# Optimization experiments

Hardware: AMD Instinct MI355X
Metric: run time of the kernel (lower is better)

The kernel has to match this reference:

```python
import jax, jax.numpy as jnp
import numpy as np

F = 256       # in_src/in_dst feature dim (feat_dict)
HID = 256     # hidden_dim
K = 16        # sampled neighbors per dst node (fixed fan-out)
N_REVIEW = 16384
N_USER = 65536
N_PRODUCT = 65536
EPS = 1e-5


def setup_inputs() -> dict:
    key = jax.random.key(0)
    ks = jax.random.split(key, 24)
    rn = lambda k, shape, s=0.05: jax.random.normal(k, shape, jnp.float32) * s
    inp = {
        'x_user': jax.random.normal(ks[0], (N_USER, F), jnp.float32),
        'x_product': jax.random.normal(ks[1], (N_PRODUCT, F), jnp.float32),
        'x_review': jax.random.normal(ks[2], (N_REVIEW, F), jnp.float32),
        'nbr_user': jax.random.randint(ks[3], (N_REVIEW, K), 0, N_USER),
        'nbr_product': jax.random.randint(ks[4], (N_REVIEW, K), 0, N_PRODUCT),
    }
    i = 5
    for pre in ('u_', 'p_'):
        inp[pre + 'Wih'] = rn(ks[i], (4 * F, F)); i += 1      # LSTM input weights (gates i,f,g,o)
        inp[pre + 'Whh'] = rn(ks[i], (4 * F, F)); i += 1      # LSTM hidden weights
        inp[pre + 'bih'] = jnp.zeros((4 * F,), jnp.float32)
        inp[pre + 'bhh'] = jnp.zeros((4 * F,), jnp.float32)
        inp[pre + 'Wself'] = rn(ks[i], (HID, F)); i += 1      # SAGEConv fc_self
        inp[pre + 'Wneigh'] = rn(ks[i], (HID, F)); i += 1     # SAGEConv fc_neigh
        inp[pre + 'bconv'] = jnp.zeros((HID,), jnp.float32)   # SAGEConv bias
    inp['ln_g'] = jnp.ones((HID,), jnp.float32)
    inp['ln_b'] = jnp.zeros((HID,), jnp.float32)
    inp['bn_g'] = jnp.ones((HID,), jnp.float32)
    inp['bn_b'] = jnp.zeros((HID,), jnp.float32)
    inp['W1'] = rn(ks[i], (HID, HID)); i += 1
    inp['b1'] = jnp.zeros((HID,), jnp.float32)
    inp['W2'] = rn(ks[i], (2, HID)); i += 1
    inp['b2'] = jnp.zeros((2,), jnp.float32)
    return inp


def _lstm_last(x, Wih, Whh, bih, bhh):
    # x: [N, K, F] neighbor sequences; returns final hidden state [N, F]
    n, _, f = x.shape
    b = bih + bhh
    def step(carry, xt):  # xt: [N, F]
        h, c = carry
        gates = xt @ Wih.T + h @ Whh.T + b  # [N, 4F]
        ig, fg, gg, og = jnp.split(gates, 4, axis=-1)
        c = jax.nn.sigmoid(fg) * c + jax.nn.sigmoid(ig) * jnp.tanh(gg)
        h = jax.nn.sigmoid(og) * jnp.tanh(c)
        return (h, c), None
    h0 = jnp.zeros((n, f), x.dtype)
    (h, _), _ = jax.lax.scan(step, (h0, h0), jnp.swapaxes(x, 0, 1))
    return h


def _sage_rel(x_src, x_dst, nbr, Wih, Whh, bih, bhh, Wself, Wneigh, bconv):
    # gather neighbor features [N_dst, K, F] (feat_drop is identity at eval)
    nb = x_src[nbr]
    h_neigh = _lstm_last(nb, Wih, Whh, bih, bhh)            # [N_dst, F]
    rst = x_dst @ Wself.T + h_neigh @ Wneigh.T + bconv       # [N_dst, HID]
    return jax.nn.gelu(rst, approximate=False)               # activation=nn.GELU()


def reference(x_user, x_product, x_review, nbr_user, nbr_product,
              u_Wih, u_Whh, u_bih, u_bhh, u_Wself, u_Wneigh, u_bconv,
              p_Wih, p_Whh, p_bih, p_bhh, p_Wself, p_Wneigh, p_bconv,
              ln_g, ln_b, bn_g, bn_b, W1, b1, W2, b2):
    # HeteroGraphConv(aggregate='sum') over the two relations into 'review'
    h = (_sage_rel(x_user, x_review, nbr_user, u_Wih, u_Whh, u_bih, u_bhh,
                   u_Wself, u_Wneigh, u_bconv)
         + _sage_rel(x_product, x_review, nbr_product, p_Wih, p_Whh, p_bih, p_bhh,
                     p_Wself, p_Wneigh, p_bconv))
    # LayerNorm
    mu = jnp.mean(h, axis=-1, keepdims=True)
    var = jnp.var(h, axis=-1, keepdims=True)
    h = (h - mu) * jax.lax.rsqrt(var + EPS) * ln_g + ln_b
    # clf head: Dropout (identity at eval) -> BatchNorm1d (batch stats) -> MLP
    bm = jnp.mean(h, axis=0, keepdims=True)
    bv = jnp.var(h, axis=0, keepdims=True)
    h = (h - bm) * jax.lax.rsqrt(bv + EPS) * bn_g + bn_b
    h = jax.nn.gelu(h @ W1.T + b1, approximate=False)
    return h @ W2.T + b2  # [N_REVIEW, 2]
```

## Files before the change

### kernel.cpp

```cpp
#include <hip/hip_runtime.h>
#include <math.h>

#define NREV 16384
#define NUSER 65536
#define NPROD 65536
#define KNBR 16
#define LDK 72

typedef __attribute__((ext_vector_type(8))) short short8;
typedef __attribute__((ext_vector_type(4))) float f32x4;
typedef unsigned short u16;

__device__ __forceinline__ u16 f2bf(float f){
  union { float f; unsigned u; } x; x.f = f;
  unsigned r = x.u + 0x7fffu + ((x.u >> 16) & 1u);
  return (u16)(r >> 16);
}
__device__ __forceinline__ float bf2f(u16 u){
  union { unsigned u; float f; } x; x.u = ((unsigned)u) << 16;
  return x.f;
}
__device__ __forceinline__ float fexp2(float x){ return __builtin_amdgcn_exp2f(x); }
__device__ __forceinline__ float frcp(float x){ return __builtin_amdgcn_rcpf(x); }
#define LOG2E 1.4426950408889634f
__device__ __forceinline__ float sigf(float x){ return frcp(1.f + fexp2(-LOG2E*x)); }
__device__ __forceinline__ float tanh_fast(float x){ return 1.f - 2.f*frcp(1.f + fexp2(2.f*LOG2E*x)); }
__device__ __forceinline__ float gelu_fast(float x){
  float u = 0.7978845608f*x*(1.f + 0.044715f*x*x);
  return 0.5f*x*(1.f + tanh_fast(u));
}

__global__ void cvt_kernel(const float* __restrict__ src, u16* __restrict__ dst, int n4){
  int i = blockIdx.x*256 + threadIdx.x;
  if(i < n4){
    float4 v = reinterpret_cast<const float4*>(src)[i];
    ushort4 o; o.x=f2bf(v.x); o.y=f2bf(v.y); o.z=f2bf(v.z); o.w=f2bf(v.w);
    reinterpret_cast<ushort4*>(dst)[i] = o;
  }
}

__global__ void pack_lstm_kernel(const float* __restrict__ Wihp, const float* __restrict__ Whhp,
                                 const float* __restrict__ bihp, const float* __restrict__ bhhp,
                                 u16* __restrict__ Bpp, float* __restrict__ bpp){
  int n = blockIdx.x;
  int g = n & 3, j = n >> 2;
  int m = g*256 + j;
  int k = threadIdx.x;
  Bpp[(size_t)n*512 + k]       = f2bf(Wihp[(size_t)m*256 + k]);
  Bpp[(size_t)n*512 + 256 + k] = f2bf(Whhp[(size_t)m*256 + k]);
  if(k == 0) bpp[n] = bihp[m] + bhhp[m];
}

__global__ void pack_sage_kernel(const float* __restrict__ Wselfp, const float* __restrict__ Wneighp,
                                 u16* __restrict__ Bsp){
  int n = blockIdx.x;
  int k = threadIdx.x;
  Bsp[(size_t)n*512 + k]       = f2bf(Wselfp[(size_t)n*256 + k]);
  Bsp[(size_t)n*512 + 256 + k] = f2bf(Wneighp[(size_t)n*256 + k]);
}

__global__ __launch_bounds__(256) void xw_kernel(
    const float* __restrict__ x, const u16* __restrict__ Bp,
    const float* __restrict__ bp, u16* __restrict__ xwout)
{
  __shared__ u16 sA[128*LDK];
  __shared__ u16 sB[128*LDK];
  int tid = threadIdx.x;
  int nt = blockIdx.x, rt = blockIdx.y;
  f32x4 acc[4][4];
  #pragma unroll
  for(int i=0;i<4;++i)
    #pragma unroll
    for(int j=0;j<4;++j) acc[i][j] = (f32x4){0.f,0.f,0.f,0.f};
  int lane = tid & 63, w = tid >> 6, wr = w >> 1, wc = w & 1;
  int ci = tid & 7, r0 = tid >> 3;
  int rrow = lane & 15, kb = (lane >> 4) * 8;

  for(int kt=0; kt<4; ++kt){
    __syncthreads();
    #pragma unroll
    for(int pp=0; pp<4; ++pp){
      int row = pp*32 + r0;
      const float* srcA = x + (size_t)(rt*128 + row)*256 + kt*64 + ci*8;
      float4 a0 = *(const float4*)srcA;
      float4 a1 = *(const float4*)(srcA + 4);
      short8 s;
      s[0]=f2bf(a0.x); s[1]=f2bf(a0.y); s[2]=f2bf(a0.z); s[3]=f2bf(a0.w);
      s[4]=f2bf(a1.x); s[5]=f2bf(a1.y); s[6]=f2bf(a1.z); s[7]=f2bf(a1.w);
      *(short8*)&sA[row*LDK + ci*8] = s;
      const u16* srcB = Bp + (size_t)(nt*128 + row)*512 + kt*64;
      *(short8*)&sB[row*LDK + ci*8] = *(const short8*)(srcB + ci*8);
    }
    __syncthreads();
    #pragma unroll
    for(int kk=0; kk<2; ++kk){
      short8 af[4], bfv[4];
      #pragma unroll
      for(int ni=0;ni<4;++ni) af[ni]  = *(const short8*)&sB[(wc*64+ni*16+rrow)*LDK + kk*32 + kb];
      #pragma unroll
      for(int mi=0;mi<4;++mi) bfv[mi] = *(const short8*)&sA[(wr*64+mi*16+rrow)*LDK + kk*32 + kb];
      #pragma unroll
      for(int ni=0;ni<4;++ni)
        #pragma unroll
        for(int mi=0;mi<4;++mi)
          acc[ni][mi] = __builtin_amdgcn_mfma_f32_16x16x32_bf16(af[ni], bfv[mi], acc[ni][mi], 0, 0, 0);
    }
  }
  #pragma unroll
  for(int mi=0;mi<4;++mi){
    size_t node = (size_t)(rt*128 + wr*64 + mi*16 + rrow);
    u16* dst = xwout + node*1024;
    #pragma unroll
    for(int ni=0;ni<4;++ni){
      int n0 = nt*128 + wc*64 + ni*16 + (lane>>4)*4;
      float4 bv = *(const float4*)&bp[n0];
      ushort4 o;
      o.x = f2bf(acc[ni][mi][0] + bv.x);
      o.y = f2bf(acc[ni][mi][1] + bv.y);
      o.z = f2bf(acc[ni][mi][2] + bv.z);
      o.w = f2bf(acc[ni][mi][3] + bv.w);
      *(ushort4*)(dst + n0) = o;
    }
  }
}

__global__ __launch_bounds__(256, 3) void lstm_step3_kernel(
    const u16* __restrict__ xw, const int* __restrict__ nbr, int t,
    const u16* __restrict__ Bh,
    const u16* __restrict__ hin, u16* __restrict__ hout, float* __restrict__ cT)
{
  __shared__ u16 sA[128*LDK];
  __shared__ u16 sB[128*LDK];
  int tid = threadIdx.x;
  int rt = blockIdx.x, nt = blockIdx.y;
  int lane = tid & 63, w = tid >> 6, wr = w >> 1, wc = w & 1;
  int ci = tid & 7, r0 = tid >> 3;
  int rrow = lane & 15, lhi = lane >> 4, kb = lhi * 8;

  int node[4];
  #pragma unroll
  for(int mi=0;mi<4;++mi)
    node[mi] = nbr[(size_t)(rt*128 + wr*64 + mi*16 + rrow)*KNBR + t];
  ushort4 xv[4][4];
  #pragma unroll
  for(int mi=0;mi<4;++mi)
    #pragma unroll
    for(int ni=0;ni<4;++ni){
      int n0 = nt*128 + wc*64 + ni*16 + lhi*4;
      xv[mi][ni] = *(const ushort4*)(xw + (size_t)node[mi]*1024 + n0);
    }

  f32x4 acc[4][4];
  #pragma unroll
  for(int i=0;i<4;++i)
    #pragma unroll
    for(int j=0;j<4;++j) acc[i][j] = (f32x4){0.f,0.f,0.f,0.f};

  if(t > 0){
    for(int kt=0; kt<4; ++kt){
      __syncthreads();
      #pragma unroll
      for(int pp=0; pp<4; ++pp){
        int row = pp*32 + r0;
        *(short8*)&sA[row*LDK + ci*8] =
          *(const short8*)(hin + (size_t)(rt*128 + row)*256 + kt*64 + ci*8);
        *(short8*)&sB[row*LDK + ci*8] =
          *(const short8*)(Bh + (size_t)(nt*128 + row)*512 + kt*64 + ci*8);
      }
      __syncthreads();
      #pragma unroll
      for(int kk=0; kk<2; ++kk){
        short8 af[4], bfv[4];
        #pragma unroll
        for(int ni=0;ni<4;++ni) af[ni]  = *(const short8*)&sB[(wc*64+ni*16+rrow)*LDK + kk*32 + kb];
        #pragma unroll
        for(int mi=0;mi<4;++mi) bfv[mi] = *(const short8*)&sA[(wr*64+mi*16+rrow)*LDK + kk*32 + kb];
        #pragma unroll
        for(int ni=0;ni<4;++ni)
          #pragma unroll
          for(int mi=0;mi<4;++mi)
            acc[ni][mi] = __builtin_amdgcn_mfma_f32_16x16x32_bf16(af[ni], bfv[mi], acc[ni][mi], 0, 0, 0);
      }
    }
  }

  float cvv[4][4];
  #pragma unroll
  for(int mi=0;mi<4;++mi)
    #pragma unroll
    for(int ni=0;ni<4;++ni){
      cvv[mi][ni] = 0.f;
      if(t > 0){
        int j = nt*32 + wc*16 + ni*4 + lhi;
        cvv[mi][ni] = cT[(size_t)j*NREV + rt*128 + wr*64 + mi*16 + rrow];
      }
    }

  #pragma unroll
  for(int mi=0;mi<4;++mi){
    int rg = rt*128 + wr*64 + mi*16 + rrow;
    #pragma unroll
    for(int ni=0;ni<4;++ni){
      int j = nt*32 + wc*16 + ni*4 + lhi;
      float ig = bf2f(xv[mi][ni].x) + acc[ni][mi][0];
      float fg = bf2f(xv[mi][ni].y) + acc[ni][mi][1];
      float gg = bf2f(xv[mi][ni].z) + acc[ni][mi][2];
      float og = bf2f(xv[mi][ni].w) + acc[ni][mi][3];
      float cn = sigf(fg)*cvv[mi][ni] + sigf(ig)*tanh_fast(gg);
      cT[(size_t)j*NREV + rg] = cn;
      hout[(size_t)rg*256 + j] = f2bf(sigf(og)*tanh_fast(cn));
    }
  }
}

template<int MODE>
__global__ __launch_bounds__(256) void gemm_act_kernel(
    const u16* __restrict__ A0, const u16* __restrict__ A1,
    const u16* __restrict__ Bp, const float* __restrict__ bias,
    float* __restrict__ outF, u16* __restrict__ outH)
{
  constexpr int KT   = (MODE == 2) ? 4 : 8;
  constexpr int KTOT = KT * 64;
  __shared__ u16 sA[128*LDK];
  __shared__ u16 sB[128*LDK];
  int tid = threadIdx.x;
  int rt = blockIdx.x, nt = blockIdx.y;
  f32x4 acc[4][4];
  #pragma unroll
  for(int i=0;i<4;++i)
    #pragma unroll
    for(int j=0;j<4;++j) acc[i][j] = (f32x4){0.f,0.f,0.f,0.f};
  int lane = tid & 63, w = tid >> 6, wr = w >> 1, wc = w & 1;
  int ci = tid & 7, r0 = tid >> 3;
  int rrow = lane & 15, kb = (lane >> 4) * 8;

  for(int kt=0; kt<KT; ++kt){
    __syncthreads();
    #pragma unroll
    for(int pp=0; pp<4; ++pp){
      int row = pp*32 + r0;
      const u16* srcA = (kt < 4)
        ? (A0 + ((size_t)(rt*128 + row))*256 + kt*64)
        : (A1 + ((size_t)(rt*128 + row))*256 + (kt-4)*64);
      *(short8*)&sA[row*LDK + ci*8] = *(const short8*)(srcA + ci*8);
      const u16* srcB = Bp + ((size_t)(nt*128 + row))*KTOT + kt*64;
      *(short8*)&sB[row*LDK + ci*8] = *(const short8*)(srcB + ci*8);
    }
    __syncthreads();
    #pragma unroll
    for(int kk=0; kk<2; ++kk){
      short8 af[4], bfv[4];
      #pragma unroll
      for(int mi=0;mi<4;++mi) af[mi] = *(const short8*)&sA[(wr*64+mi*16+rrow)*LDK + kk*32 + kb];
      #pragma unroll
      for(int ni=0;ni<4;++ni) bfv[ni] = *(const short8*)&sB[(wc*64+ni*16+rrow)*LDK + kk*32 + kb];
      #pragma unroll
      for(int mi=0;mi<4;++mi)
        #pragma unroll
        for(int ni=0;ni<4;++ni)
          acc[mi][ni] = __builtin_amdgcn_mfma_f32_16x16x32_bf16(af[mi], bfv[ni], acc[mi][ni], 0, 0, 0);
    }
  }
  #pragma unroll
  for(int mi=0;mi<4;++mi)
    #pragma unroll
    for(int ni=0;ni<4;++ni){
      int col  = nt*128 + wc*64 + ni*16 + rrow;
      int rowb = rt*128 + wr*64 + mi*16 + (lane>>4)*4;
      float bv = bias[col];
      #pragma unroll
      for(int q=0;q<4;++q){
        float x = acc[mi][ni][q] + bv;
        float gl = gelu_fast(x);
        size_t idx = (size_t)(rowb+q)*256 + col;
        if(MODE == 0)      outF[idx] = gl;
        else if(MODE == 1) outF[idx] += gl;
        else               outH[idx] = f2bf(gl);
      }
    }
}

__global__ void ln_kernel(const float* __restrict__ hs, const float* __restrict__ g,
                          const float* __restrict__ b, u16* __restrict__ hlnp){
  int w = threadIdx.x >> 6, lane = threadIdx.x & 63;
  int r = blockIdx.x*4 + w;
  const float* row = hs + (size_t)r*256;
  float4 v = *(const float4*)(row + lane*4);
  float s  = v.x+v.y+v.z+v.w;
  float ss = v.x*v.x + v.y*v.y + v.z*v.z + v.w*v.w;
  #pragma unroll
  for(int d=1; d<64; d<<=1){ s += __shfl_xor(s, d, 64); ss += __shfl_xor(ss, d, 64); }
  float mu  = s  * (1.f/256.f);
  float var = ss * (1.f/256.f) - mu*mu;
  float rs  = rsqrtf(var + 1e-5f);
  float4 gv = *(const float4*)(g + lane*4);
  float4 bv = *(const float4*)(b + lane*4);
  ushort4 o;
  o.x = f2bf((v.x-mu)*rs*gv.x + bv.x);
  o.y = f2bf((v.y-mu)*rs*gv.y + bv.y);
  o.z = f2bf((v.z-mu)*rs*gv.z + bv.z);
  o.w = f2bf((v.w-mu)*rs*gv.w + bv.w);
  *(ushort4*)(hlnp + (size_t)r*256 + lane*4) = o;
}

__global__ void colstats_kernel(const u16* __restrict__ hlnp, float* __restrict__ cs, float* __restrict__ cq){
  int cix = threadIdx.x;
  size_t rb = (size_t)blockIdx.x * 128;
  float s=0.f, q=0.f;
  for(int rr=0; rr<128; ++rr){
    float v = bf2f(hlnp[(rb+rr)*256 + cix]);
    s += v; q += v*v;
  }
  atomicAdd(&cs[cix], s);
  atomicAdd(&cq[cix], q);
}

__global__ void fold_kernel(const float* __restrict__ cs, const float* __restrict__ cq,
                            const float* __restrict__ bng, const float* __restrict__ bnb,
                            const float* __restrict__ W1p, const float* __restrict__ b1p,
                            u16* __restrict__ W1fp, float* __restrict__ b1fp){
  __shared__ float sS[256], sT[256];
  int cix = threadIdx.x;
  float bm = cs[cix] * (1.f/16384.f);
  float bv = cq[cix] * (1.f/16384.f) - bm*bm;
  float s  = bng[cix] * rsqrtf(bv + 1e-5f);
  float tt = bnb[cix] - bm*s;
  sS[cix]=s; sT[cix]=tt;
  __syncthreads();
  float a = b1p[cix];
  for(int k=0;k<256;++k){
    float wv = W1p[(size_t)cix*256 + k];
    W1fp[(size_t)cix*256 + k] = f2bf(wv * sS[k]);
    a += wv * sT[k];
  }
  b1fp[cix] = a;
}

__global__ void head_kernel(const u16* __restrict__ z, const float* __restrict__ W2p,
                            const float* __restrict__ b2p, float* __restrict__ outp){
  int w = threadIdx.x >> 6, lane = threadIdx.x & 63;
  int r = blockIdx.x*4 + w;
  const u16* zr = z + (size_t)r*256;
  ushort4 v = *(const ushort4*)(zr + lane*4);
  float z0=bf2f(v.x), z1v=bf2f(v.y), z2=bf2f(v.z), z3=bf2f(v.w);
  float4 wa = *(const float4*)(W2p + lane*4);
  float4 wb = *(const float4*)(W2p + 256 + lane*4);
  float p0 = z0*wa.x + z1v*wa.y + z2*wa.z + z3*wa.w;
  float p1 = z0*wb.x + z1v*wb.y + z2*wb.z + z3*wb.w;
  #pragma unroll
  for(int d=1; d<64; d<<=1){ p0 += __shfl_xor(p0,d,64); p1 += __shfl_xor(p1,d,64); }
  if(lane == 0){
    outp[(size_t)r*2]   = p0 + b2p[0];
    outp[(size_t)r*2+1] = p1 + b2p[1];
  }
}

extern "C" void kernel_launch(void* const* d_in, const int* in_sizes, int n_in,
                              void* d_out, int out_size, void* d_ws, size_t ws_size,
                              hipStream_t stream){
  (void)in_sizes; (void)n_in; (void)out_size;
  const float* x_user    = (const float*)d_in[0];
  const float* x_product = (const float*)d_in[1];
  const float* x_review  = (const float*)d_in[2];
  const int*   nbr_user  = (const int*)d_in[3];
  const int*   nbr_prod  = (const int*)d_in[4];
  const float* Wih[2]    = {(const float*)d_in[5],  (const float*)d_in[12]};
  const float* Whh[2]    = {(const float*)d_in[6],  (const float*)d_in[13]};
  const float* bih[2]    = {(const float*)d_in[7],  (const float*)d_in[14]};
  const float* bhh[2]    = {(const float*)d_in[8],  (const float*)d_in[15]};
  const float* Wself[2]  = {(const float*)d_in[9],  (const float*)d_in[16]};
  const float* Wneigh[2] = {(const float*)d_in[10], (const float*)d_in[17]};
  const float* bconv[2]  = {(const float*)d_in[11], (const float*)d_in[18]};
  const float* ln_g=(const float*)d_in[19], *ln_b=(const float*)d_in[20];
  const float* bn_g=(const float*)d_in[21], *bn_b=(const float*)d_in[22];
  const float* W1=(const float*)d_in[23], *b1=(const float*)d_in[24];
  const float* W2=(const float*)d_in[25], *b2=(const float*)d_in[26];
  float* out = (float*)d_out;

  char* base = (char*)d_ws;
  size_t off = 0;
  auto alloc = [&](size_t bytes)->char* { char* r = base + off; off += (bytes + 255) & ~(size_t)255; return r; };
  u16*   xr   = (u16*)  alloc((size_t)NREV*256*2);
  float* hsum = (float*)alloc((size_t)NREV*256*4);
  u16*   Bp[2]; Bp[0]=(u16*)alloc(1024*512*2); Bp[1]=(u16*)alloc(1024*512*2);
  float* bp[2]; bp[0]=(float*)alloc(4096);     bp[1]=(float*)alloc(4096);
  u16*   Bs[2]; Bs[0]=(u16*)alloc(256*512*2);  Bs[1]=(u16*)alloc(256*512*2);
  float* csum = (float*)alloc(1024);
  float* csq  = (float*)alloc(1024);
  u16*   W1f  = (u16*)  alloc(256*256*2);
  float* b1f  = (float*)alloc(1024);
  u16*   hA   = (u16*)  alloc((size_t)NREV*256*2);
  u16*   hB   = (u16*)  alloc((size_t)NREV*256*2);
  float* cT   = (float*)alloc((size_t)NREV*256*4);
  u16*   xW   = (u16*)  alloc((size_t)NUSER*1024*2);
  if(off > ws_size) return;
  u16* hln = hA;
  u16* z1  = hB;

  cvt_kernel<<<dim3(4096),256,0,stream>>>(x_review, xr, NREV*256/4);
  for(int rel=0; rel<2; ++rel){
    pack_lstm_kernel<<<dim3(1024),256,0,stream>>>(Wih[rel],Whh[rel],bih[rel],bhh[rel],Bp[rel],bp[rel]);
    pack_sage_kernel<<<dim3(256), 256,0,stream>>>(Wself[rel],Wneigh[rel],Bs[rel]);
  }
  hipMemsetAsync(csum, 0, 1024, stream);
  hipMemsetAsync(csq,  0, 1024, stream);

  u16* hfin[2];
  for(int rel=0; rel<2; ++rel){
    const float* xs = rel ? x_product : x_user;
    const int*   nb = rel ? nbr_prod  : nbr_user;
    xw_kernel<<<dim3(8,512),256,0,stream>>>(xs, Bp[rel], bp[rel], xW);
    u16 *hin = hB, *hout = hA;
    for(int t=0; t<KNBR; ++t){
      lstm_step3_kernel<<<dim3(128,8),256,0,stream>>>(xW, nb, t, Bp[rel] + 256, hin, hout, cT);
      u16* tmp = hin; hin = hout; hout = tmp;
    }
    hfin[rel] = hin;
    if(rel == 0)
      gemm_act_kernel<0><<<dim3(128,2),256,0,stream>>>(xr, hfin[0], Bs[0], bconv[0], hsum, nullptr);
    else
      gemm_act_kernel<1><<<dim3(128,2),256,0,stream>>>(xr, hfin[1], Bs[1], bconv[1], hsum, nullptr);
  }

  ln_kernel<<<dim3(4096),256,0,stream>>>(hsum, ln_g, ln_b, hln);
  colstats_kernel<<<dim3(128),256,0,stream>>>(hln, csum, csq);
  fold_kernel<<<dim3(1),256,0,stream>>>(csum, csq, bn_g, bn_b, W1, b1, W1f, b1f);
  gemm_act_kernel<2><<<dim3(128,2),256,0,stream>>>(hln, nullptr, W1f, b1f, nullptr, z1);
  head_kernel<<<dim3(4096),256,0,stream>>>(z1, W2, b2, out);
}
```

Measured before the change: 1.278 ms.

## Load MFMA fragments directly from global memory, drop LDS staging in GEMMs

The xw and per-step LSTM GEMMs no longer stage tiles through shared memory with syncthreads. Each lane reads its bf16 fragments straight from global memory, relying on L1/L2 reuse. The neighbor features are first converted to bf16 by a separate pass into workspace aliased over the h/c buffers. The LSTM grid order is swapped so blocks sharing the same hidden-state rows launch together, and the occupancy hint is removed. The cost is strided, less coalesced global loads and more cache traffic in exchange for removing barriers and LDS round-trips.

```diff
diff --git a/kernel.cpp b/kernel.cpp
--- a/kernel.cpp
+++ b/kernel.cpp
@@ -60,51 +60,38 @@
 }
 
 __global__ __launch_bounds__(256) void xw_kernel(
-    const float* __restrict__ x, const u16* __restrict__ Bp,
+    const u16* __restrict__ xb, const u16* __restrict__ Bp,
     const float* __restrict__ bp, u16* __restrict__ xwout)
 {
-  __shared__ u16 sA[128*LDK];
-  __shared__ u16 sB[128*LDK];
   int tid = threadIdx.x;
   int nt = blockIdx.x, rt = blockIdx.y;
+  int lane = tid & 63, w = tid >> 6, wr = w >> 1, wc = w & 1;
+  int rrow = lane & 15, lhi = lane >> 4, kb = lhi*8;
+
   f32x4 acc[4][4];
   #pragma unroll
   for(int i=0;i<4;++i)
     #pragma unroll
     for(int j=0;j<4;++j) acc[i][j] = (f32x4){0.f,0.f,0.f,0.f};
-  int lane = tid & 63, w = tid >> 6, wr = w >> 1, wc = w & 1;
-  int ci = tid & 7, r0 = tid >> 3;
-  int rrow = lane & 15, kb = (lane >> 4) * 8;
-
-  for(int kt=0; kt<4; ++kt){
-    __syncthreads();
-    #pragma unroll
-    for(int pp=0; pp<4; ++pp){
-      int row = pp*32 + r0;
-      const float* srcA = x + (size_t)(rt*128 + row)*256 + kt*64 + ci*8;
-      float4 a0 = *(const float4*)srcA;
-      float4 a1 = *(const float4*)(srcA + 4);
-      short8 s;
-      s[0]=f2bf(a0.x); s[1]=f2bf(a0.y); s[2]=f2bf(a0.z); s[3]=f2bf(a0.w);
-      s[4]=f2bf(a1.x); s[5]=f2bf(a1.y); s[6]=f2bf(a1.z); s[7]=f2bf(a1.w);
-      *(short8*)&sA[row*LDK + ci*8] = s;
-      const u16* srcB = Bp + (size_t)(nt*128 + row)*512 + kt*64;
-      *(short8*)&sB[row*LDK + ci*8] = *(const short8*)(srcB + ci*8);
-    }
-    __syncthreads();
-    #pragma unroll
-    for(int kk=0; kk<2; ++kk){
-      short8 af[4], bfv[4];
-      #pragma unroll
-      for(int ni=0;ni<4;++ni) af[ni]  = *(const short8*)&sB[(wc*64+ni*16+rrow)*LDK + kk*32 + kb];
-      #pragma unroll
-      for(int mi=0;mi<4;++mi) bfv[mi] = *(const short8*)&sA[(wr*64+mi*16+rrow)*LDK + kk*32 + kb];
-      #pragma unroll
-      for(int ni=0;ni<4;++ni)
-        #pragma unroll
-        for(int mi=0;mi<4;++mi)
-          acc[ni][mi] = __builtin_amdgcn_mfma_f32_16x16x32_bf16(af[ni], bfv[mi], acc[ni][mi], 0, 0, 0);
-    }
+
+  const u16* arow[4]; const u16* brow[4];
+  #pragma unroll
+  for(int mi=0;mi<4;++mi) arow[mi] = xb + (size_t)(rt*128 + wr*64 + mi*16 + rrow)*256 + kb;
+  #pragma unroll
+  for(int ni=0;ni<4;++ni) brow[ni] = Bp + (size_t)(nt*128 + wc*64 + ni*16 + rrow)*512 + kb;
+
+  #pragma unroll 2
+  for(int k0=0; k0<8; ++k0){
+    short8 af[4], bfv[4];
+    #pragma unroll
+    for(int mi=0;mi<4;++mi) af[mi]  = *(const short8*)(arow[mi] + k0*32);
+    #pragma unroll
+    for(int ni=0;ni<4;++ni) bfv[ni] = *(const short8*)(brow[ni] + k0*32);
+    #pragma unroll
+    for(int ni=0;ni<4;++ni)
+      #pragma unroll
+      for(int mi=0;mi<4;++mi)
+        acc[ni][mi] = __builtin_amdgcn_mfma_f32_16x16x32_bf16(bfv[ni], af[mi], acc[ni][mi], 0, 0, 0);
   }
   #pragma unroll
   for(int mi=0;mi<4;++mi){
@@ -112,7 +99,7 @@
     u16* dst = xwout + node*1024;
     #pragma unroll
     for(int ni=0;ni<4;++ni){
-      int n0 = nt*128 + wc*64 + ni*16 + (lane>>4)*4;
+      int n0 = nt*128 + wc*64 + ni*16 + lhi*4;
       float4 bv = *(const float4*)&bp[n0];
       ushort4 o;
       o.x = f2bf(acc[ni][mi][0] + bv.x);
@@ -124,18 +111,15 @@
   }
 }
 
-__global__ __launch_bounds__(256, 3) void lstm_step3_kernel(
+__global__ __launch_bounds__(256) void lstm_step4_kernel(
     const u16* __restrict__ xw, const int* __restrict__ nbr, int t,
     const u16* __restrict__ Bh,
     const u16* __restrict__ hin, u16* __restrict__ hout, float* __restrict__ cT)
 {
-  __shared__ u16 sA[128*LDK];
-  __shared__ u16 sB[128*LDK];
   int tid = threadIdx.x;
-  int rt = blockIdx.x, nt = blockIdx.y;
+  int nt = blockIdx.x, rt = blockIdx.y;
   int lane = tid & 63, w = tid >> 6, wr = w >> 1, wc = w & 1;
-  int ci = tid & 7, r0 = tid >> 3;
-  int rrow = lane & 15, lhi = lane >> 4, kb = lhi * 8;
+  int rrow = lane & 15, lhi = lane >> 4, kb = lhi*8;
 
   int node[4];
   #pragma unroll
@@ -145,10 +129,8 @@
   #pragma unroll
   for(int mi=0;mi<4;++mi)
     #pragma unroll
-    for(int ni=0;ni<4;++ni){
-      int n0 = nt*128 + wc*64 + ni*16 + lhi*4;
-      xv[mi][ni] = *(const ushort4*)(xw + (size_t)node[mi]*1024 + n0);
-    }
+    for(int ni=0;ni<4;++ni)
+      xv[mi][ni] = *(const ushort4*)(xw + (size_t)node[mi]*1024 + nt*128 + wc*64 + ni*16 + lhi*4);
 
   f32x4 acc[4][4];
   #pragma unroll
@@ -157,30 +139,23 @@
     for(int j=0;j<4;++j) acc[i][j] = (f32x4){0.f,0.f,0.f,0.f};
 
   if(t > 0){
-    for(int kt=0; kt<4; ++kt){
-      __syncthreads();
-      #pragma unroll
-      for(int pp=0; pp<4; ++pp){
-        int row = pp*32 + r0;
-        *(short8*)&sA[row*LDK + ci*8] =
-          *(const short8*)(hin + (size_t)(rt*128 + row)*256 + kt*64 + ci*8);
-        *(short8*)&sB[row*LDK + ci*8] =
-          *(const short8*)(Bh + (size_t)(nt*128 + row)*512 + kt*64 + ci*8);
-      }
-      __syncthreads();
-      #pragma unroll
-      for(int kk=0; kk<2; ++kk){
-        short8 af[4], bfv[4];
+    const u16* arow[4]; const u16* brow[4];
+    #pragma unroll
+    for(int mi=0;mi<4;++mi) arow[mi] = hin + (size_t)(rt*128 + wr*64 + mi*16 + rrow)*256 + kb;
+    #pragma unroll
+    for(int ni=0;ni<4;++ni) brow[ni] = Bh + (size_t)(nt*128 + wc*64 + ni*16 + rrow)*512 + kb;
+    #pragma unroll 2
+    for(int k0=0; k0<8; ++k0){
+      short8 af[4], bfv[4];
+      #pragma unroll
+      for(int mi=0;mi<4;++mi) af[mi]  = *(const short8*)(arow[mi] + k0*32);
+      #pragma unroll
+      for(int ni=0;ni<4;++ni) bfv[ni] = *(const short8*)(brow[ni] + k0*32);
+      #pragma unroll
+      for(int ni=0;ni<4;++ni)
         #pragma unroll
-        for(int ni=0;ni<4;++ni) af[ni]  = *(const short8*)&sB[(wc*64+ni*16+rrow)*LDK + kk*32 + kb];
-        #pragma unroll
-        for(int mi=0;mi<4;++mi) bfv[mi] = *(const short8*)&sA[(wr*64+mi*16+rrow)*LDK + kk*32 + kb];
-        #pragma unroll
-        for(int ni=0;ni<4;++ni)
-          #pragma unroll
-          for(int mi=0;mi<4;++mi)
-            acc[ni][mi] = __builtin_amdgcn_mfma_f32_16x16x32_bf16(af[ni], bfv[mi], acc[ni][mi], 0, 0, 0);
-      }
+        for(int mi=0;mi<4;++mi)
+          acc[ni][mi] = __builtin_amdgcn_mfma_f32_16x16x32_bf16(bfv[ni], af[mi], acc[ni][mi], 0, 0, 0);
     }
   }
 
@@ -394,8 +369,9 @@
   float* cT   = (float*)alloc((size_t)NREV*256*4);
   u16*   xW   = (u16*)  alloc((size_t)NUSER*1024*2);
   if(off > ws_size) return;
-  u16* hln = hA;
-  u16* z1  = hB;
+  u16* xcvt = hA;
+  u16* hln  = hA;
+  u16* z1   = hB;
 
   cvt_kernel<<<dim3(4096),256,0,stream>>>(x_review, xr, NREV*256/4);
   for(int rel=0; rel<2; ++rel){
@@ -405,21 +381,20 @@
   hipMemsetAsync(csum, 0, 1024, stream);
   hipMemsetAsync(csq,  0, 1024, stream);
 
-  u16* hfin[2];
   for(int rel=0; rel<2; ++rel){
     const float* xs = rel ? x_product : x_user;
     const int*   nb = rel ? nbr_prod  : nbr_user;
-    xw_kernel<<<dim3(8,512),256,0,stream>>>(xs, Bp[rel], bp[rel], xW);
+    cvt_kernel<<<dim3(16384),256,0,stream>>>(xs, xcvt, NUSER*256/4);
+    xw_kernel<<<dim3(8,512),256,0,stream>>>(xcvt, Bp[rel], bp[rel], xW);
     u16 *hin = hB, *hout = hA;
     for(int t=0; t<KNBR; ++t){
-      lstm_step3_kernel<<<dim3(128,8),256,0,stream>>>(xW, nb, t, Bp[rel] + 256, hin, hout, cT);
+      lstm_step4_kernel<<<dim3(8,128),256,0,stream>>>(xW, nb, t, Bp[rel] + 256, hin, hout, cT);
       u16* tmp = hin; hin = hout; hout = tmp;
     }
-    hfin[rel] = hin;
     if(rel == 0)
-      gemm_act_kernel<0><<<dim3(128,2),256,0,stream>>>(xr, hfin[0], Bs[0], bconv[0], hsum, nullptr);
+      gemm_act_kernel<0><<<dim3(128,2),256,0,stream>>>(xr, hin, Bs[0], bconv[0], hsum, nullptr);
     else
-      gemm_act_kernel<1><<<dim3(128,2),256,0,stream>>>(xr, hfin[1], Bs[1], bconv[1], hsum, nullptr);
+      gemm_act_kernel<1><<<dim3(128,2),256,0,stream>>>(xr, hin, Bs[1], bconv[1], hsum, nullptr);
   }
 
   ln_kernel<<<dim3(4096),256,0,stream>>>(hsum, ln_g, ln_b, hln);
```

New measurement: 1.907 ms. 49.1% more time.

## Widen LSTM step tiles, store cell state in bf16, pre-convert x

Applied to the files above, without the earlier changes.

The LSTM step kernel now uses 512-thread blocks that each compute a 128-row by 256-gate-column tile. This halves how often each hidden-state tile is reloaded across the gate dimension. The cell state buffer is stored as bf16 instead of fp32, and its load is moved up next to the gathered x*W load to cut memory traffic and latency per step. The source features are converted to bf16 in a separate cvt pass before xw_kernel. That pass writes into the hA region, overrunning it into hB and cT, which are not in use at that point. Keeping the cell state in bf16 adds rounding error that builds up over the 16 recurrent steps.

```diff
diff --git a/kernel.cpp b/kernel.cpp
--- a/kernel.cpp
+++ b/kernel.cpp
@@ -60,7 +60,7 @@
 }
 
 __global__ __launch_bounds__(256) void xw_kernel(
-    const float* __restrict__ x, const u16* __restrict__ Bp,
+    const u16* __restrict__ xb, const u16* __restrict__ Bp,
     const float* __restrict__ bp, u16* __restrict__ xwout)
 {
   __shared__ u16 sA[128*LDK];
@@ -74,22 +74,17 @@
     for(int j=0;j<4;++j) acc[i][j] = (f32x4){0.f,0.f,0.f,0.f};
   int lane = tid & 63, w = tid >> 6, wr = w >> 1, wc = w & 1;
   int ci = tid & 7, r0 = tid >> 3;
-  int rrow = lane & 15, kb = (lane >> 4) * 8;
+  int rrow = lane & 15, lhi = lane >> 4, kb = lhi * 8;
 
   for(int kt=0; kt<4; ++kt){
     __syncthreads();
     #pragma unroll
     for(int pp=0; pp<4; ++pp){
       int row = pp*32 + r0;
-      const float* srcA = x + (size_t)(rt*128 + row)*256 + kt*64 + ci*8;
-      float4 a0 = *(const float4*)srcA;
-      float4 a1 = *(const float4*)(srcA + 4);
-      short8 s;
-      s[0]=f2bf(a0.x); s[1]=f2bf(a0.y); s[2]=f2bf(a0.z); s[3]=f2bf(a0.w);
-      s[4]=f2bf(a1.x); s[5]=f2bf(a1.y); s[6]=f2bf(a1.z); s[7]=f2bf(a1.w);
-      *(short8*)&sA[row*LDK + ci*8] = s;
-      const u16* srcB = Bp + (size_t)(nt*128 + row)*512 + kt*64;
-      *(short8*)&sB[row*LDK + ci*8] = *(const short8*)(srcB + ci*8);
+      *(short8*)&sA[row*LDK + ci*8] =
+        *(const short8*)(xb + (size_t)(rt*128 + row)*256 + kt*64 + ci*8);
+      *(short8*)&sB[row*LDK + ci*8] =
+        *(const short8*)(Bp + (size_t)(nt*128 + row)*512 + kt*64 + ci*8);
     }
     __syncthreads();
     #pragma unroll
@@ -112,7 +107,7 @@
     u16* dst = xwout + node*1024;
     #pragma unroll
     for(int ni=0;ni<4;++ni){
-      int n0 = nt*128 + wc*64 + ni*16 + (lane>>4)*4;
+      int n0 = nt*128 + wc*64 + ni*16 + lhi*4;
       float4 bv = *(const float4*)&bp[n0];
       ushort4 o;
       o.x = f2bf(acc[ni][mi][0] + bv.x);
@@ -124,30 +119,35 @@
   }
 }
 
-__global__ __launch_bounds__(256, 3) void lstm_step3_kernel(
+__global__ __launch_bounds__(512) void lstm_step5_kernel(
     const u16* __restrict__ xw, const int* __restrict__ nbr, int t,
     const u16* __restrict__ Bh,
-    const u16* __restrict__ hin, u16* __restrict__ hout, float* __restrict__ cT)
+    const u16* __restrict__ hin, u16* __restrict__ hout, u16* __restrict__ cT)
 {
   __shared__ u16 sA[128*LDK];
-  __shared__ u16 sB[128*LDK];
+  __shared__ u16 sB[256*LDK];
   int tid = threadIdx.x;
-  int rt = blockIdx.x, nt = blockIdx.y;
-  int lane = tid & 63, w = tid >> 6, wr = w >> 1, wc = w & 1;
-  int ci = tid & 7, r0 = tid >> 3;
-  int rrow = lane & 15, lhi = lane >> 4, kb = lhi * 8;
+  int nt = blockIdx.x, rt = blockIdx.y;
+  int lane = tid & 63, w = tid >> 6;
+  int wrr = w & 1, wnn = w >> 1;
+  int rrow = lane & 15, lhi = lane >> 4, kb = lhi*8;
 
   int node[4];
   #pragma unroll
   for(int mi=0;mi<4;++mi)
-    node[mi] = nbr[(size_t)(rt*128 + wr*64 + mi*16 + rrow)*KNBR + t];
+    node[mi] = nbr[(size_t)(rt*128 + wrr*64 + mi*16 + rrow)*KNBR + t];
   ushort4 xv[4][4];
+  u16 cv[4][4];
   #pragma unroll
   for(int mi=0;mi<4;++mi)
     #pragma unroll
     for(int ni=0;ni<4;++ni){
-      int n0 = nt*128 + wc*64 + ni*16 + lhi*4;
+      int n0 = nt*256 + wnn*64 + ni*16 + lhi*4;
       xv[mi][ni] = *(const ushort4*)(xw + (size_t)node[mi]*1024 + n0);
+      if(t > 0)
+        cv[mi][ni] = cT[(size_t)(n0>>2)*NREV + rt*128 + wrr*64 + mi*16 + rrow];
+      else
+        cv[mi][ni] = 0;
     }
 
   f32x4 acc[4][4];
@@ -157,24 +157,26 @@
     for(int j=0;j<4;++j) acc[i][j] = (f32x4){0.f,0.f,0.f,0.f};
 
   if(t > 0){
+    int ra = tid >> 2, ca = (tid & 3) * 2;
+    int rb = tid >> 1, cb = (tid & 1) * 4;
     for(int kt=0; kt<4; ++kt){
       __syncthreads();
       #pragma unroll
-      for(int pp=0; pp<4; ++pp){
-        int row = pp*32 + r0;
-        *(short8*)&sA[row*LDK + ci*8] =
-          *(const short8*)(hin + (size_t)(rt*128 + row)*256 + kt*64 + ci*8);
-        *(short8*)&sB[row*LDK + ci*8] =
-          *(const short8*)(Bh + (size_t)(nt*128 + row)*512 + kt*64 + ci*8);
-      }
+      for(int q=0;q<2;++q)
+        *(short8*)&sA[ra*LDK + (ca+q)*8] =
+          *(const short8*)(hin + (size_t)(rt*128 + ra)*256 + kt*64 + (ca+q)*8);
+      #pragma unroll
+      for(int q=0;q<4;++q)
+        *(short8*)&sB[rb*LDK + (cb+q)*8] =
+          *(const short8*)(Bh + (size_t)(nt*256 + rb)*512 + kt*64 + (cb+q)*8);
       __syncthreads();
       #pragma unroll
       for(int kk=0; kk<2; ++kk){
         short8 af[4], bfv[4];
         #pragma unroll
-        for(int ni=0;ni<4;++ni) af[ni]  = *(const short8*)&sB[(wc*64+ni*16+rrow)*LDK + kk*32 + kb];
+        for(int ni=0;ni<4;++ni) af[ni]  = *(const short8*)&sB[(wnn*64+ni*16+rrow)*LDK + kk*32 + kb];
         #pragma unroll
-        for(int mi=0;mi<4;++mi) bfv[mi] = *(const short8*)&sA[(wr*64+mi*16+rrow)*LDK + kk*32 + kb];
+        for(int mi=0;mi<4;++mi) bfv[mi] = *(const short8*)&sA[(wrr*64+mi*16+rrow)*LDK + kk*32 + kb];
         #pragma unroll
         for(int ni=0;ni<4;++ni)
           #pragma unroll
@@ -184,30 +186,18 @@
     }
   }
 
-  float cvv[4][4];
-  #pragma unroll
-  for(int mi=0;mi<4;++mi)
+  #pragma unroll
+  for(int mi=0;mi<4;++mi){
+    int rg = rt*128 + wrr*64 + mi*16 + rrow;
     #pragma unroll
     for(int ni=0;ni<4;++ni){
-      cvv[mi][ni] = 0.f;
-      if(t > 0){
-        int j = nt*32 + wc*16 + ni*4 + lhi;
-        cvv[mi][ni] = cT[(size_t)j*NREV + rt*128 + wr*64 + mi*16 + rrow];
-      }
-    }
-
-  #pragma unroll
-  for(int mi=0;mi<4;++mi){
-    int rg = rt*128 + wr*64 + mi*16 + rrow;
-    #pragma unroll
-    for(int ni=0;ni<4;++ni){
-      int j = nt*32 + wc*16 + ni*4 + lhi;
+      int j = nt*64 + wnn*16 + ni*4 + lhi;
       float ig = bf2f(xv[mi][ni].x) + acc[ni][mi][0];
       float fg = bf2f(xv[mi][ni].y) + acc[ni][mi][1];
       float gg = bf2f(xv[mi][ni].z) + acc[ni][mi][2];
       float og = bf2f(xv[mi][ni].w) + acc[ni][mi][3];
-      float cn = sigf(fg)*cvv[mi][ni] + sigf(ig)*tanh_fast(gg);
-      cT[(size_t)j*NREV + rg] = cn;
+      float cn = sigf(fg)*bf2f(cv[mi][ni]) + sigf(ig)*tanh_fast(gg);
+      cT[(size_t)j*NREV + rg] = f2bf(cn);
       hout[(size_t)rg*256 + j] = f2bf(sigf(og)*tanh_fast(cn));
     }
   }
@@ -389,13 +379,14 @@
   float* csq  = (float*)alloc(1024);
   u16*   W1f  = (u16*)  alloc(256*256*2);
   float* b1f  = (float*)alloc(1024);
-  u16*   hA   = (u16*)  alloc((size_t)NREV*256*2);
-  u16*   hB   = (u16*)  alloc((size_t)NREV*256*2);
-  float* cT   = (float*)alloc((size_t)NREV*256*4);
-  u16*   xW   = (u16*)  alloc((size_t)NUSER*1024*2);
+  u16*   hA    = (u16*)alloc((size_t)NREV*256*2);
+  u16*   hB    = (u16*)alloc((size_t)NREV*256*2);
+  u16*   cT    = (u16*)alloc((size_t)NREV*256*4);
+  u16*   xW    = (u16*)alloc((size_t)NUSER*1024*2);
   if(off > ws_size) return;
-  u16* hln = hA;
-  u16* z1  = hB;
+  u16* xcvt = hA;
+  u16* hln  = hA;
+  u16* z1   = hB;
 
   cvt_kernel<<<dim3(4096),256,0,stream>>>(x_review, xr, NREV*256/4);
   for(int rel=0; rel<2; ++rel){
@@ -405,21 +396,20 @@
   hipMemsetAsync(csum, 0, 1024, stream);
   hipMemsetAsync(csq,  0, 1024, stream);
 
-  u16* hfin[2];
   for(int rel=0; rel<2; ++rel){
     const float* xs = rel ? x_product : x_user;
     const int*   nb = rel ? nbr_prod  : nbr_user;
-    xw_kernel<<<dim3(8,512),256,0,stream>>>(xs, Bp[rel], bp[rel], xW);
+    cvt_kernel<<<dim3(16384),256,0,stream>>>(xs, xcvt, NUSER*256/4);
+    xw_kernel<<<dim3(8,512),256,0,stream>>>(xcvt, Bp[rel], bp[rel], xW);
     u16 *hin = hB, *hout = hA;
     for(int t=0; t<KNBR; ++t){
-      lstm_step3_kernel<<<dim3(128,8),256,0,stream>>>(xW, nb, t, Bp[rel] + 256, hin, hout, cT);
+      lstm_step5_kernel<<<dim3(4,128),512,0,stream>>>(xW, nb, t, Bp[rel] + 256, hin, hout, cT);
       u16* tmp = hin; hin = hout; hout = tmp;
     }
-    hfin[rel] = hin;
     if(rel == 0)
-      gemm_act_kernel<0><<<dim3(128,2),256,0,stream>>>(xr, hfin[0], Bs[0], bconv[0], hsum, nullptr);
+      gemm_act_kernel<0><<<dim3(128,2),256,0,stream>>>(xr, hin, Bs[0], bconv[0], hsum, nullptr);
     else
-      gemm_act_kernel<1><<<dim3(128,2),256,0,stream>>>(xr, hfin[1], Bs[1], bconv[1], hsum, nullptr);
+      gemm_act_kernel<1><<<dim3(128,2),256,0,stream>>>(xr, hin, Bs[1], bconv[1], hsum, nullptr);
   }
 
   ln_kernel<<<dim3(4096),256,0,stream>>>(hsum, ln_g, ln_b, hln);
```

Result: slower. 1.542 ms (+20.6%).
